# Optimization experiments

Hardware: AMD Instinct MI355X
Metric: run time of the kernel (lower is better)

Reference implementation:

```python
import jax, jax.numpy as jnp
import numpy as np

NUM_GRAPHS = 3000
L = 7        # num_gc_layers
D = 256      # dims * power
DIMS = 64
POWER = 4
MSG_EPS = 1e-7
LN_EPS = 1e-5


def layer_norm(x, g, b):
    mu = jnp.mean(x, axis=-1, keepdims=True)
    var = jnp.var(x, axis=-1, keepdims=True)
    return (x - mu) * jax.lax.rsqrt(var + LN_EPS) * g + b


def gen_conv(h, src, dst, edge_emb, w, b, n_nodes):
    # GENConv (OGB DeeperGCN), aggr='add', mlp_layers=1:
    #   msg = relu(x_j + e) + eps ; agg = scatter_add ; out = Linear(x + agg)
    msg = jax.nn.relu(h[src] + edge_emb) + MSG_EPS      # [E, D]
    agg = jax.ops.segment_sum(msg, dst, num_segments=n_nodes)
    return (h + agg) @ w + b


def mlp_vn(v, w1, b1, g1, be1, w2, b2, g2, be2):
    # MLP([D, D, D], norm='layer'): Lin -> LN -> ReLU -> Lin -> LN -> ReLU
    v = jax.nn.relu(layer_norm(v @ w1 + b1, g1, be1))
    v = jax.nn.relu(layer_norm(v @ w2 + b2, g2, be2))
    return v


def _forward(x, edge_attr, edge_index, batch, atom_emb, bond_emb, vn_emb,
             gcn_w, gcn_b, norm_g, norm_b, ffn_w, ffn_b,
             vn_w1, vn_b1, vn_g1, vn_be1, vn_w2, vn_b2, vn_g2, vn_be2):
    N = x.shape[0]
    # AtomEncoder / BondEncoder: sum of per-feature embedding gathers
    h = atom_emb[jnp.arange(9), x].sum(axis=1)              # [N, D]
    edge_emb = bond_emb[jnp.arange(3), edge_attr].sum(axis=1)  # [E, D]
    h_init = h

    vn = jnp.broadcast_to(vn_emb[0], (NUM_GRAPHS, D))        # Embedding(1, D) row 0
    h = h + vn[batch]

    src, dst = edge_index[0], edge_index[1]
    out = []
    h = gen_conv(h, src, dst, edge_emb, gcn_w[0], gcn_b[0], N)
    out.append(h @ ffn_w[0] + ffn_b[0])

    for layer in range(1, L):
        h2 = jax.nn.relu(layer_norm(h, norm_g[layer - 1], norm_b[layer - 1]))
        vn_tmp = jax.ops.segment_sum(h2, batch, num_segments=NUM_GRAPHS) + vn
        j = layer - 1
        vn = mlp_vn(vn_tmp, vn_w1[j], vn_b1[j], vn_g1[j], vn_be1[j],
                    vn_w2[j], vn_b2[j], vn_g2[j], vn_be2[j])  # dropout: eval mode -> identity
        h2 = h2 + vn[batch]
        h = gen_conv(h2, src, dst, edge_emb, gcn_w[layer], gcn_b[layer], N) + h
        out.append(h @ ffn_w[layer] + ffn_b[layer])

    h_graph = jnp.concatenate([out[p] for p in range(POWER)], axis=-1)  # [N, 4*64]
    return h_graph, h_init


def setup_inputs() -> dict:
    key = jax.random.key(0)
    ks = jax.random.split(key, 12)
    N, E = 100000, 300000
    s = 0.05
    return dict(
        x=jax.random.randint(ks[0], (N, 9), 0, 64),
        edge_attr=jax.random.randint(ks[1], (E, 3), 0, 8),
        edge_index=jax.random.randint(ks[2], (2, E), 0, N),
        batch=jnp.sort(jax.random.randint(ks[3], (N,), 0, NUM_GRAPHS)),
        atom_emb=jax.random.normal(ks[4], (9, 64, D)) * s,
        bond_emb=jax.random.normal(ks[5], (3, 8, D)) * s,
        vn_emb=jnp.zeros((1, D)),
        gcn_w=jax.random.normal(ks[6], (L, D, D)) * s,
        gcn_b=jnp.zeros((L, D)),
        norm_g=jnp.ones((L, D)),
        norm_b=jnp.zeros((L, D)),
        ffn_w=jax.random.normal(ks[7], (L, D, DIMS)) * s,
        ffn_b=jnp.zeros((L, DIMS)),
        vn_w1=jax.random.normal(ks[8], (L - 1, D, D)) * s,
        vn_b1=jnp.zeros((L - 1, D)),
        vn_g1=jnp.ones((L - 1, D)),
        vn_be1=jnp.zeros((L - 1, D)),
        vn_w2=jax.random.normal(ks[9], (L - 1, D, D)) * s,
        vn_b2=jnp.zeros((L - 1, D)),
        vn_g2=jnp.ones((L - 1, D)),
        vn_be2=jnp.zeros((L - 1, D)),
    )


def reference(x, edge_attr, edge_index, batch, atom_emb, bond_emb, vn_emb,
              gcn_w, gcn_b, norm_g, norm_b, ffn_w, ffn_b,
              vn_w1, vn_b1, vn_g1, vn_be1, vn_w2, vn_b2, vn_g2, vn_be2):
    return _forward(x, edge_attr, edge_index, batch, atom_emb, bond_emb, vn_emb,
                    gcn_w, gcn_b, norm_g, norm_b, ffn_w, ffn_b,
                    vn_w1, vn_b1, vn_g1, vn_be1, vn_w2, vn_b2, vn_g2, vn_be2)
```

## Files before the change

### kernel.cpp

```cpp
#include <hip/hip_runtime.h>
#include <hip/hip_bf16.h>

#define G_NUM 3000

typedef unsigned short u16;
typedef unsigned int u32;

typedef short s16x8 __attribute__((ext_vector_type(8)));
typedef float f32x4 __attribute__((ext_vector_type(4)));

__device__ __forceinline__ float bf2f(u16 u) {
    union { u32 i; float f; } v; v.i = ((u32)u) << 16; return v.f;
}
__device__ __forceinline__ u16 f2bf(float f) {
    union { float f; u32 i; } v; v.f = f;
    u32 r = (v.i + 0x7FFFu + ((v.i >> 16) & 1u)) >> 16;
    return (u16)r;
}
__device__ __forceinline__ float ldf(const void* p, size_t i, int bf) {
    return bf ? bf2f(((const u16*)p)[i]) : ((const float*)p)[i];
}

__device__ __forceinline__ void gl_lds16(const void* g, void* l) {
    __builtin_amdgcn_global_load_lds(
        (const __attribute__((address_space(1))) void*)g,
        (__attribute__((address_space(3))) void*)l, 16, 0, 0);
}

__global__ void k_flag(const u32* __restrict__ norm_g_u32, int* __restrict__ flag) {
    if (threadIdx.x == 0 && blockIdx.x == 0)
        *flag = (norm_g_u32[0] == 0x3F803F80u) ? 1 : 0;
}

__global__ void k_hist(const int* __restrict__ ei, int* __restrict__ cnt, int E) {
    int e = blockIdx.x * blockDim.x + threadIdx.x;
    if (e < E) atomicAdd(&cnt[ei[E + e]], 1);
}

__global__ __launch_bounds__(256) void k_scan_part(const int* __restrict__ cnt,
                                                   int* __restrict__ epos,
                                                   int* __restrict__ part, int N) {
    __shared__ int sh[256];
    int t = threadIdx.x;
    int base = blockIdx.x * 1024 + t * 4;
    int c0 = (base + 0 < N) ? cnt[base + 0] : 0;
    int c1 = (base + 1 < N) ? cnt[base + 1] : 0;
    int c2 = (base + 2 < N) ? cnt[base + 2] : 0;
    int c3 = (base + 3 < N) ? cnt[base + 3] : 0;
    int s4 = c0 + c1 + c2 + c3;
    sh[t] = s4;
    __syncthreads();
    for (int off = 1; off < 256; off <<= 1) {
        int v = (t >= off) ? sh[t - off] : 0;
        __syncthreads();
        sh[t] += v;
        __syncthreads();
    }
    int excl = sh[t] - s4;
    if (base + 0 < N) epos[base + 0] = excl;
    if (base + 1 < N) epos[base + 1] = excl + c0;
    if (base + 2 < N) epos[base + 2] = excl + c0 + c1;
    if (base + 3 < N) epos[base + 3] = excl + c0 + c1 + c2;
    if (t == 255) part[blockIdx.x] = sh[255];
}

__global__ __launch_bounds__(256) void k_scan_top(int* __restrict__ part, int NB) {
    __shared__ int sh[256];
    int t = threadIdx.x;
    int v = (t < NB) ? part[t] : 0;
    sh[t] = v;
    __syncthreads();
    for (int off = 1; off < 256; off <<= 1) {
        int u = (t >= off) ? sh[t - off] : 0;
        __syncthreads();
        sh[t] += u;
        __syncthreads();
    }
    if (t < NB) part[t] = sh[t] - v;
}

__global__ __launch_bounds__(256) void k_scan_fin(int* __restrict__ epos,
                                                  const int* __restrict__ part, int N) {
    int add = part[blockIdx.x];
    int base = blockIdx.x * 1024 + threadIdx.x * 4;
#pragma unroll
    for (int i = 0; i < 4; ++i)
        if (base + i < N) epos[base + i] += add;
}

__global__ void k_scatter(const int* __restrict__ ei, int* __restrict__ epos,
                          int* __restrict__ elist, int E) {
    int e = blockIdx.x * blockDim.x + threadIdx.x;
    if (e < E) {
        int p = atomicAdd(&epos[ei[E + e]], 1);
        elist[p] = e;
    }
}

__global__ void k_atom(const int* __restrict__ x, const void* __restrict__ atom_emb,
                       const void* __restrict__ vn_emb, const int* __restrict__ flagp,
                       float* __restrict__ h, int N) {
    int id = blockIdx.x * blockDim.x + threadIdx.x;
    if (id >= N * 64) return;
    int bf = *flagp;
    int n = id >> 6, d = (id & 63) << 2;
    float s0 = 0.f, s1 = 0.f, s2 = 0.f, s3 = 0.f;
#pragma unroll
    for (int f = 0; f < 9; ++f) {
        size_t row = (size_t)(f * 64 + x[n * 9 + f]) * 256 + d;
        if (bf) {
            ushort4 v = *(const ushort4*)((const u16*)atom_emb + row);
            s0 += bf2f(v.x); s1 += bf2f(v.y); s2 += bf2f(v.z); s3 += bf2f(v.w);
        } else {
            float4 v = *(const float4*)((const float*)atom_emb + row);
            s0 += v.x; s1 += v.y; s2 += v.z; s3 += v.w;
        }
    }
    float4 o = { s0 + ldf(vn_emb, d, bf),     s1 + ldf(vn_emb, d + 1, bf),
                 s2 + ldf(vn_emb, d + 2, bf), s3 + ldf(vn_emb, d + 3, bf) };
    *(float4*)(h + (size_t)n * 256 + d) = o;
}

__global__ void k_hinit(const int* __restrict__ x, const void* __restrict__ atom_emb,
                        const int* __restrict__ flagp, void* __restrict__ d_out_v, int N) {
    int id = blockIdx.x * blockDim.x + threadIdx.x;
    if (id >= N * 64) return;
    int bf = *flagp;
    int n = id >> 6, d = (id & 63) << 2;
    float s0 = 0.f, s1 = 0.f, s2 = 0.f, s3 = 0.f;
#pragma unroll
    for (int f = 0; f < 9; ++f) {
        size_t row = (size_t)(f * 64 + x[n * 9 + f]) * 256 + d;
        if (bf) {
            ushort4 v = *(const ushort4*)((const u16*)atom_emb + row);
            s0 += bf2f(v.x); s1 += bf2f(v.y); s2 += bf2f(v.z); s3 += bf2f(v.w);
        } else {
            float4 v = *(const float4*)((const float*)atom_emb + row);
            s0 += v.x; s1 += v.y; s2 += v.z; s3 += v.w;
        }
    }
    size_t idx = (size_t)N * 256 + (size_t)n * 256 + d;
    if (bf) {
        ushort4 o = { f2bf(s0), f2bf(s1), f2bf(s2), f2bf(s3) };
        *(ushort4*)((u16*)d_out_v + idx) = o;
    } else {
        float4 o = { s0, s1, s2, s3 };
        *(float4*)((float*)d_out_v + idx) = o;
    }
}

__global__ void k_init_vn(const void* __restrict__ vn_emb, const int* __restrict__ flagp,
                          float* __restrict__ vn) {
    int id = blockIdx.x * blockDim.x + threadIdx.x;
    if (id >= G_NUM * 256) return;
    vn[id] = ldf(vn_emb, id & 255, *flagp);
}

__global__ __launch_bounds__(256) void k_agg(
    const int* __restrict__ ei, const int* __restrict__ eattr,
    const int* __restrict__ elist, const int* __restrict__ epos,
    const int* __restrict__ cnt, const void* __restrict__ bond_emb,
    const int* __restrict__ flagp, const float* __restrict__ h,
    const void* __restrict__ d_out_v, u16* __restrict__ xh, u16* __restrict__ xl,
    const float* __restrict__ vnarr, const int* __restrict__ batch,
    int layer0, int E, int N) {
    int bf = *flagp;
    int wv = threadIdx.x >> 6, lane = threadIdx.x & 63;
    int n = blockIdx.x * 4 + wv;
    if (n >= N) return;
    int d = lane << 2;
    size_t ND = (size_t)N * 256;
    int end = epos[n];
    int deg = cnt[n];
    int start = end - deg;

    float i0, i1, i2, i3;
    if (layer0) {
        float4 iv = *(const float4*)(h + (size_t)n * 256 + d);
        i0 = iv.x; i1 = iv.y; i2 = iv.z; i3 = iv.w;
    } else {
        float4 vv = *(const float4*)(vnarr + (size_t)batch[n] * 256 + d);
        if (bf) {
            ushort4 iv = *(const ushort4*)((const u16*)d_out_v + ND + (size_t)n * 256 + d);
            i0 = bf2f(iv.x) + vv.x; i1 = bf2f(iv.y) + vv.y;
            i2 = bf2f(iv.z) + vv.z; i3 = bf2f(iv.w) + vv.w;
        } else {
            float4 iv = *(const float4*)((const float*)d_out_v + ND + (size_t)n * 256 + d);
            i0 = iv.x + vv.x; i1 = iv.y + vv.y; i2 = iv.z + vv.z; i3 = iv.w + vv.w;
        }
    }

    float a0 = 0.f, a1 = 0.f, a2 = 0.f, a3 = 0.f;
    for (int b0i = 0; b0i < deg; b0i += 64) {
        int m = min(64, deg - b0i);
        int src = 0, bsrc = 0, c0 = 0, c1 = 0, c2 = 0;
        if (lane < m) {
            int e = elist[start + b0i + lane];
            src = ei[e];
            c0 = eattr[e * 3]; c1 = eattr[e * 3 + 1]; c2 = eattr[e * 3 + 2];
            if (!layer0) bsrc = batch[src];
        }
        for (int j = 0; j < m; ++j) {
            int sj = __shfl(src, j);
            int q0 = __shfl(c0, j), q1 = __shfl(c1, j), q2 = __shfl(c2, j);
            float e0, e1, e2, e3;
            if (bf) {
                const u16* bp = (const u16*)bond_emb;
                ushort4 w0 = *(const ushort4*)(bp + (size_t)q0 * 256 + d);
                ushort4 w1 = *(const ushort4*)(bp + (size_t)(8 + q1) * 256 + d);
                ushort4 w2 = *(const ushort4*)(bp + (size_t)(16 + q2) * 256 + d);
                e0 = bf2f(w0.x) + bf2f(w1.x) + bf2f(w2.x);
                e1 = bf2f(w0.y) + bf2f(w1.y) + bf2f(w2.y);
                e2 = bf2f(w0.z) + bf2f(w1.z) + bf2f(w2.z);
                e3 = bf2f(w0.w) + bf2f(w1.w) + bf2f(w2.w);
            } else {
                const float* bp = (const float*)bond_emb;
                float4 w0 = *(const float4*)(bp + (size_t)q0 * 256 + d);
                float4 w1 = *(const float4*)(bp + (size_t)(8 + q1) * 256 + d);
                float4 w2 = *(const float4*)(bp + (size_t)(16 + q2) * 256 + d);
                e0 = w0.x + w1.x + w2.x; e1 = w0.y + w1.y + w2.y;
                e2 = w0.z + w1.z + w2.z; e3 = w0.w + w1.w + w2.w;
            }
            float h0, h1, h2v, h3;
            if (layer0) {
                float4 hs = *(const float4*)(h + (size_t)sj * 256 + d);
                h0 = hs.x; h1 = hs.y; h2v = hs.z; h3 = hs.w;
            } else {
                int bj = __shfl(bsrc, j);
                float4 vv = *(const float4*)(vnarr + (size_t)bj * 256 + d);
                if (bf) {
                    ushort4 hs = *(const ushort4*)((const u16*)d_out_v + ND + (size_t)sj * 256 + d);
                    h0 = bf2f(hs.x) + vv.x; h1 = bf2f(hs.y) + vv.y;
                    h2v = bf2f(hs.z) + vv.z; h3 = bf2f(hs.w) + vv.w;
                } else {
                    float4 hs = *(const float4*)((const float*)d_out_v + ND + (size_t)sj * 256 + d);
                    h0 = hs.x + vv.x; h1 = hs.y + vv.y; h2v = hs.z + vv.z; h3 = hs.w + vv.w;
                }
            }
            a0 += fmaxf(h0 + e0, 0.f) + 1e-7f;
            a1 += fmaxf(h1 + e1, 0.f) + 1e-7f;
            a2 += fmaxf(h2v + e2, 0.f) + 1e-7f;
            a3 += fmaxf(h3 + e3, 0.f) + 1e-7f;
        }
    }

    float o0 = i0 + a0, o1 = i1 + a1, o2 = i2 + a2, o3 = i3 + a3;
    u16 h0 = f2bf(o0), h1 = f2bf(o1), h2 = f2bf(o2), h3 = f2bf(o3);
    ushort4 hv = { h0, h1, h2, h3 };
    size_t base = (size_t)n * 256 + d;
    *(ushort4*)(xh + base) = hv;
    if (!bf) {
        ushort4 lv = { f2bf(o0 - bf2f(h0)), f2bf(o1 - bf2f(h1)),
                       f2bf(o2 - bf2f(h2)), f2bf(o3 - bf2f(h3)) };
        *(ushort4*)(xl + base) = lv;
    }
}

__global__ void k_prep_w(const void* __restrict__ gcn_w, const void* __restrict__ ffn_w,
                         const int* __restrict__ flagp,
                         u16* __restrict__ cwh, u16* __restrict__ cwl,
                         u16* __restrict__ fwh, u16* __restrict__ fwl) {
    int bf = *flagp;
    int t = blockIdx.x * blockDim.x + threadIdx.x;
    const int CONVT = 4 * 8 * 16 * 64;
    const int FFNT  = 4 * 8 * 4 * 64;
    if (t >= CONVT + FFNT) return;
    bool isc = t < CONVT;
    int u = isc ? t : t - CONVT;
    int lane = u & 63;
    int g = lane >> 4, c16 = lane & 15;
    int ncf = isc ? 16 : 4;
    int fid = u >> 6;
    int cf = fid % ncf;
    int kk = (fid / ncf) & 7;
    int layer = fid / (ncf * 8);
    int ncol = isc ? 256 : 64;
    int col = cf * 16 + c16;
    const void* W = isc ? gcn_w : ffn_w;
    u16* oh = isc ? cwh : fwh;
    u16* ol = isc ? cwl : fwl;
    size_t lbase = (size_t)layer * 256 * ncol;
    size_t o = (size_t)u * 8;
#pragma unroll
    for (int i = 0; i < 8; ++i) {
        int k = kk * 32 + g * 8 + i;
        float v = ldf(W, lbase + (size_t)k * ncol + col, bf);
        u16 hv = f2bf(v);
        oh[o + i] = hv;
        ol[o + i] = f2bf(v - bf2f(hv));
    }
}

__global__ __launch_bounds__(512, 8) void k_mconv(
    const u16* __restrict__ Ah, const u16* __restrict__ Al,
    const u16* __restrict__ cwh, const u16* __restrict__ cwl,
    const u16* __restrict__ fwh, const u16* __restrict__ fwl,
    const void* __restrict__ cbias, const void* __restrict__ fbias,
    const void* __restrict__ res, void* __restrict__ hOut,
    void* __restrict__ d_out_v, const int* __restrict__ flagp,
    const void* __restrict__ ng, const void* __restrict__ nb,
    int cboff, int fboff, int col_off, int goff, int N) {
    __shared__ __align__(16) u16 Shi[32 * 256];
    __shared__ __align__(16) u16 Slo[32 * 256];
    __shared__ float redS[8][2][16];
    __shared__ float redQ[8][2][16];
    int bf = *flagp;
    int t = threadIdx.x;
    int wv = t >> 6, lane = t & 63;
    int g = lane >> 4, c16 = lane & 15;
    int r0 = blockIdx.x * 32;
    size_t ND = (size_t)N * 256;

    {
        int l5 = lane >> 5;
        int cb = (lane & 31) * 16;
#pragma unroll
        for (int j = 0; j < 2; ++j) {
            int rowl = wv * 4 + j * 2 + l5;
            int gr = r0 + rowl; if (gr > N - 1) gr = N - 1;
            int scb = cb ^ ((rowl & 7) << 4);
            const u16* sh = Ah + (size_t)gr * 256 + (scb >> 1);
            gl_lds16(sh, &Shi[wv * 1024 + j * 512]);
            if (!bf) {
                const u16* sl = Al + (size_t)gr * 256 + (scb >> 1);
                gl_lds16(sl, &Slo[wv * 1024 + j * 512]);
            }
        }
    }
    __syncthreads();

    f32x4 acc[2][2] = {};
    if (bf) {
#pragma unroll
        for (int kk = 0; kk < 8; ++kk) {
            s16x8 wh[2];
#pragma unroll
            for (int c = 0; c < 2; ++c)
                wh[c] = *(const s16x8*)(cwh + ((size_t)((kk * 16 + wv * 2 + c) * 64 + lane) * 8));
#pragma unroll
            for (int rf = 0; rf < 2; ++rf) {
                int R = rf * 16 + c16;
                int cbyte = (kk * 64 + g * 16) ^ ((R & 7) << 4);
                s16x8 ah = *(const s16x8*)((const char*)Shi + R * 512 + cbyte);
#pragma unroll
                for (int c = 0; c < 2; ++c)
                    acc[rf][c] = __builtin_amdgcn_mfma_f32_16x16x32_bf16(wh[c], ah, acc[rf][c], 0, 0, 0);
            }
        }
    } else {
#pragma unroll
        for (int kk = 0; kk < 8; ++kk) {
            s16x8 wh[2], wl[2];
#pragma unroll
            for (int c = 0; c < 2; ++c) {
                size_t off = (size_t)((kk * 16 + wv * 2 + c) * 64 + lane) * 8;
                wh[c] = *(const s16x8*)(cwh + off);
                wl[c] = *(const s16x8*)(cwl + off);
            }
#pragma unroll
            for (int rf = 0; rf < 2; ++rf) {
                int R = rf * 16 + c16;
                int cbyte = (kk * 64 + g * 16) ^ ((R & 7) << 4);
                s16x8 ah = *(const s16x8*)((const char*)Shi + R * 512 + cbyte);
                s16x8 al = *(const s16x8*)((const char*)Slo + R * 512 + cbyte);
#pragma unroll
                for (int c = 0; c < 2; ++c) {
                    acc[rf][c] = __builtin_amdgcn_mfma_f32_16x16x32_bf16(wh[c], ah, acc[rf][c], 0, 0, 0);
                    acc[rf][c] = __builtin_amdgcn_mfma_f32_16x16x32_bf16(wh[c], al, acc[rf][c], 0, 0, 0);
                    acc[rf][c] = __builtin_amdgcn_mfma_f32_16x16x32_bf16(wl[c], ah, acc[rf][c], 0, 0, 0);
                    acc[rf][c] = __builtin_amdgcn_mfma_f32_16x16x32_bf16(wl[c], al, acc[rf][c], 0, 0, 0);
                }
            }
        }
    }
    __syncthreads();

    float o[2][2][4];
#pragma unroll
    for (int rf = 0; rf < 2; ++rf) {
        int R = rf * 16 + c16;
        int r = r0 + R;
#pragma unroll
        for (int c = 0; c < 2; ++c) {
            int colb = (wv * 2 + c) * 16 + g * 4;
#pragma unroll
            for (int i = 0; i < 4; ++i)
                o[rf][c][i] = acc[rf][c][i] + ldf(cbias, cboff + colb + i, bf);
            if (res && r < N) {
                if (bf) {
                    ushort4 rv = *(const ushort4*)((const u16*)res + (size_t)r * 256 + colb);
                    o[rf][c][0] += bf2f(rv.x); o[rf][c][1] += bf2f(rv.y);
                    o[rf][c][2] += bf2f(rv.z); o[rf][c][3] += bf2f(rv.w);
                } else {
                    float4 rv = *(const float4*)((const float*)res + (size_t)r * 256 + colb);
                    o[rf][c][0] += rv.x; o[rf][c][1] += rv.y;
                    o[rf][c][2] += rv.z; o[rf][c][3] += rv.w;
                }
            }
        }
        if (hOut && r < N) {
#pragma unroll
            for (int c = 0; c < 2; ++c) {
                int colb = (wv * 2 + c) * 16 + g * 4;
                if (bf) {
                    ushort4 ov = { f2bf(o[rf][c][0]), f2bf(o[rf][c][1]),
                                   f2bf(o[rf][c][2]), f2bf(o[rf][c][3]) };
                    *(ushort4*)((u16*)hOut + (size_t)r * 256 + colb) = ov;
                } else {
                    float4 ov = { o[rf][c][0], o[rf][c][1], o[rf][c][2], o[rf][c][3] };
                    *(float4*)((float*)hOut + (size_t)r * 256 + colb) = ov;
                }
            }
        }
    }

    float mu[2], rs_[2];
    if (goff >= 0) {
#pragma unroll
        for (int rf = 0; rf < 2; ++rf) {
            float s = 0.f;
#pragma unroll
            for (int c = 0; c < 2; ++c)
#pragma unroll
                for (int i = 0; i < 4; ++i) s += o[rf][c][i];
            s += __shfl_xor(s, 16);
            s += __shfl_xor(s, 32);
            if (g == 0) redS[wv][rf][c16] = s;
        }
    }
    __syncthreads();
    if (goff >= 0) {
#pragma unroll
        for (int rf = 0; rf < 2; ++rf) {
            float s8 = 0.f;
#pragma unroll
            for (int w = 0; w < 8; ++w) s8 += redS[w][rf][c16];
            mu[rf] = s8 * (1.f / 256.f);
            float q = 0.f;
#pragma unroll
            for (int c = 0; c < 2; ++c)
#pragma unroll
                for (int i = 0; i < 4; ++i) {
                    float dv = o[rf][c][i] - mu[rf];
                    q += dv * dv;
                }
            q += __shfl_xor(q, 16);
            q += __shfl_xor(q, 32);
            if (g == 0) redQ[wv][rf][c16] = q;
        }
    }
    __syncthreads();
    if (goff >= 0) {
#pragma unroll
        for (int rf = 0; rf < 2; ++rf) {
            float q8 = 0.f;
#pragma unroll
            for (int w = 0; w < 8; ++w) q8 += redQ[w][rf][c16];
            float var = q8 * (1.f / 256.f);
            rs_[rf] = rsqrtf(fmaxf(var, 0.f) + 1e-5f);
            int r = r0 + rf * 16 + c16;
            if (r < N) {
#pragma unroll
                for (int c = 0; c < 2; ++c) {
                    int colb = (wv * 2 + c) * 16 + g * 4;
                    float v0 = fmaxf((o[rf][c][0] - mu[rf]) * rs_[rf] * ldf(ng, goff + colb, bf)     + ldf(nb, goff + colb, bf), 0.f);
                    float v1 = fmaxf((o[rf][c][1] - mu[rf]) * rs_[rf] * ldf(ng, goff + colb + 1, bf) + ldf(nb, goff + colb + 1, bf), 0.f);
                    float v2 = fmaxf((o[rf][c][2] - mu[rf]) * rs_[rf] * ldf(ng, goff + colb + 2, bf) + ldf(nb, goff + colb + 2, bf), 0.f);
                    float v3 = fmaxf((o[rf][c][3] - mu[rf]) * rs_[rf] * ldf(ng, goff + colb + 3, bf) + ldf(nb, goff + colb + 3, bf), 0.f);
                    size_t oi = ND + (size_t)r * 256 + colb;
                    if (bf) {
                        ushort4 q4 = { f2bf(v0), f2bf(v1), f2bf(v2), f2bf(v3) };
                        *(ushort4*)((u16*)d_out_v + oi) = q4;
                    } else {
                        float4 q4 = { v0, v1, v2, v3 };
                        *(float4*)((float*)d_out_v + oi) = q4;
                    }
                }
            }
        }
    }

#pragma unroll
    for (int rf = 0; rf < 2; ++rf) {
        int R = rf * 16 + c16;
#pragma unroll
        for (int c = 0; c < 2; ++c) {
            int colb = (wv * 2 + c) * 16 + g * 4;
            float o0 = o[rf][c][0], o1 = o[rf][c][1], o2 = o[rf][c][2], o3 = o[rf][c][3];
            u16 h0 = f2bf(o0), h1 = f2bf(o1), h2 = f2bf(o2), h3 = f2bf(o3);
            ushort4 hv = { h0, h1, h2, h3 };
            int cbyte = (colb * 2) ^ ((R & 7) << 4);
            *(ushort4*)((char*)Shi + R * 512 + cbyte) = hv;
            if (!bf) {
                ushort4 lv = { f2bf(o0 - bf2f(h0)), f2bf(o1 - bf2f(h1)),
                               f2bf(o2 - bf2f(h2)), f2bf(o3 - bf2f(h3)) };
                *(ushort4*)((char*)Slo + R * 512 + cbyte) = lv;
            }
        }
    }
    __syncthreads();

    f32x4 fa = {};
    {
        int rfw = wv >> 2, cfw = wv & 3;
        int R = rfw * 16 + c16;
        if (bf) {
#pragma unroll
            for (int kk = 0; kk < 8; ++kk) {
                s16x8 wh = *(const s16x8*)(fwh + ((size_t)((kk * 4 + cfw) * 64 + lane) * 8));
                int cbyte = (kk * 64 + g * 16) ^ ((R & 7) << 4);
                s16x8 ah = *(const s16x8*)((const char*)Shi + R * 512 + cbyte);
                fa = __builtin_amdgcn_mfma_f32_16x16x32_bf16(wh, ah, fa, 0, 0, 0);
            }
        } else {
#pragma unroll
            for (int kk = 0; kk < 8; ++kk) {
                size_t off = (size_t)((kk * 4 + cfw) * 64 + lane) * 8;
                s16x8 wh = *(const s16x8*)(fwh + off);
                s16x8 wl = *(const s16x8*)(fwl + off);
                int cbyte = (kk * 64 + g * 16) ^ ((R & 7) << 4);
                s16x8 ah = *(const s16x8*)((const char*)Shi + R * 512 + cbyte);
                s16x8 al = *(const s16x8*)((const char*)Slo + R * 512 + cbyte);
                fa = __builtin_amdgcn_mfma_f32_16x16x32_bf16(wh, ah, fa, 0, 0, 0);
                fa = __builtin_amdgcn_mfma_f32_16x16x32_bf16(wh, al, fa, 0, 0, 0);
                fa = __builtin_amdgcn_mfma_f32_16x16x32_bf16(wl, ah, fa, 0, 0, 0);
                fa = __builtin_amdgcn_mfma_f32_16x16x32_bf16(wl, al, fa, 0, 0, 0);
            }
        }

        int colb = cfw * 16 + g * 4;
        float b0 = ldf(fbias, fboff + colb, bf);
        float b1 = ldf(fbias, fboff + colb + 1, bf);
        float b2 = ldf(fbias, fboff + colb + 2, bf);
        float b3 = ldf(fbias, fboff + colb + 3, bf);
        int r = r0 + R;
        if (r < N) {
            float o0 = fa[0] + b0, o1 = fa[1] + b1;
            float o2 = fa[2] + b2, o3 = fa[3] + b3;
            size_t oi = (size_t)r * 256 + col_off + colb;
            if (bf) {
                ushort4 q = { f2bf(o0), f2bf(o1), f2bf(o2), f2bf(o3) };
                *(ushort4*)((u16*)d_out_v + oi) = q;
            } else {
                float4 q = { o0, o1, o2, o3 };
                *(float4*)((float*)d_out_v + oi) = q;
            }
        }
    }
}

__global__ __launch_bounds__(256) void k_vn4(
    const void* __restrict__ d_out_v, const int* __restrict__ flagp,
    const int* __restrict__ batch,
    const void* __restrict__ w1, const void* __restrict__ b1,
    const void* __restrict__ g1, const void* __restrict__ be1,
    const void* __restrict__ w2, const void* __restrict__ b2,
    const void* __restrict__ g2, const void* __restrict__ be2,
    float* __restrict__ vn, int woff, int voff, int N) {
    __shared__ float row[4][256];
    __shared__ float red[4][4];
    __shared__ __align__(16) float Ws[32][256];
    int bf = *flagp;
    int t = threadIdx.x;
    int wv = t >> 6, lane = t & 63;
    size_t ND = (size_t)N * 256;

    {
        int gi = blockIdx.x * 4 + wv;
        int lo = 0, hi = N;
        while (lo < hi) { int m = (lo + hi) >> 1; if (batch[m] < gi) lo = m + 1; else hi = m; }
        int s = lo; hi = N;
        while (lo < hi) { int m = (lo + hi) >> 1; if (batch[m] < gi + 1) lo = m + 1; else hi = m; }
        int e = lo;
        int d = lane << 2;
        float4 a = *(const float4*)(vn + (size_t)gi * 256 + d);
        for (int n = s; n < e; ++n) {
            size_t base = ND + (size_t)n * 256 + d;
            if (bf) {
                ushort4 hv = *(const ushort4*)((const u16*)d_out_v + base);
                a.x += bf2f(hv.x); a.y += bf2f(hv.y); a.z += bf2f(hv.z); a.w += bf2f(hv.w);
            } else {
                float4 hv = *(const float4*)((const float*)d_out_v + base);
                a.x += hv.x; a.y += hv.y; a.z += hv.z; a.w += hv.w;
            }
        }
        *(float4*)&row[wv][d] = a;
    }
    __syncthreads();

#pragma unroll 1
    for (int stage = 0; stage < 2; ++stage) {
        const void* W = stage ? w2 : w1;
        const void* B = stage ? b2 : b1;
        const void* G = stage ? g2 : g1;
        const void* BE = stage ? be2 : be1;
        float bb = ldf(B, voff + t, bf);
        float acc[4] = { bb, bb, bb, bb };
#pragma unroll 1
        for (int k0 = 0; k0 < 256; k0 += 32) {
            if (bf) {
                const u32* Wg = (const u32*)((const u16*)W + woff);
#pragma unroll
                for (int i = 0; i < 16; ++i) {
                    int idx = t + i * 256;
                    int k = idx >> 7, c2 = idx & 127;
                    u32 v = Wg[(size_t)(k0 + k) * 128 + c2];
                    Ws[k][2 * c2] = bf2f((u16)(v & 0xffff));
                    Ws[k][2 * c2 + 1] = bf2f((u16)(v >> 16));
                }
            } else {
                const float4* Wg = (const float4*)((const float*)W + woff);
#pragma unroll
                for (int i = 0; i < 8; ++i) {
                    int idx = t + i * 256;
                    int k = idx >> 6, c4 = idx & 63;
                    *(float4*)&Ws[k][4 * c4] = Wg[(size_t)(k0 + k) * 64 + c4];
                }
            }
            __syncthreads();
#pragma unroll
            for (int k = 0; k < 32; ++k) {
                float w = Ws[k][t];
                float r0 = row[0][k0 + k], r1 = row[1][k0 + k];
                float r2 = row[2][k0 + k], r3 = row[3][k0 + k];
                acc[0] = fmaf(r0, w, acc[0]);
                acc[1] = fmaf(r1, w, acc[1]);
                acc[2] = fmaf(r2, w, acc[2]);
                acc[3] = fmaf(r3, w, acc[3]);
            }
            __syncthreads();
        }
        float mu[4], rs_[4];
#pragma unroll
        for (int gr = 0; gr < 4; ++gr) {
            float s = acc[gr];
#pragma unroll
            for (int o = 32; o > 0; o >>= 1) s += __shfl_xor(s, o);
            if (lane == 0) red[wv][gr] = s;
        }
        __syncthreads();
#pragma unroll
        for (int gr = 0; gr < 4; ++gr)
            mu[gr] = (red[0][gr] + red[1][gr] + red[2][gr] + red[3][gr]) * (1.f / 256.f);
        __syncthreads();
#pragma unroll
        for (int gr = 0; gr < 4; ++gr) {
            float dv = acc[gr] - mu[gr];
            float q = dv * dv;
#pragma unroll
            for (int o = 32; o > 0; o >>= 1) q += __shfl_xor(q, o);
            if (lane == 0) red[wv][gr] = q;
        }
        __syncthreads();
        float gn = ldf(G, voff + t, bf), bn = ldf(BE, voff + t, bf);
#pragma unroll
        for (int gr = 0; gr < 4; ++gr) {
            float var = (red[0][gr] + red[1][gr] + red[2][gr] + red[3][gr]) * (1.f / 256.f);
            rs_[gr] = rsqrtf(fmaxf(var, 0.f) + 1e-5f);
        }
        __syncthreads();
#pragma unroll
        for (int gr = 0; gr < 4; ++gr)
            row[gr][t] = fmaxf((acc[gr] - mu[gr]) * rs_[gr] * gn + bn, 0.f);
        __syncthreads();
    }
#pragma unroll
    for (int gr = 0; gr < 4; ++gr)
        vn[(size_t)(blockIdx.x * 4 + gr) * 256 + t] = row[gr][t];
}

extern "C" void kernel_launch(void* const* d_in, const int* in_sizes, int n_in,
                              void* d_out, int out_size, void* d_ws, size_t ws_size,
                              hipStream_t stream) {
    const int* x      = (const int*)d_in[0];
    const int* eattr  = (const int*)d_in[1];
    const int* ei     = (const int*)d_in[2];
    const int* batch  = (const int*)d_in[3];
    const void* atom_emb = d_in[4];
    const void* bond_emb = d_in[5];
    const void* vn_emb   = d_in[6];
    const void* gcn_w    = d_in[7];
    const void* gcn_b    = d_in[8];
    const void* norm_g   = d_in[9];
    const void* norm_b   = d_in[10];
    const void* ffn_w    = d_in[11];
    const void* ffn_b    = d_in[12];
    const void* vn_w1    = d_in[13];
    const void* vn_b1    = d_in[14];
    const void* vn_g1    = d_in[15];
    const void* vn_be1   = d_in[16];
    const void* vn_w2    = d_in[17];
    const void* vn_b2    = d_in[18];
    const void* vn_g2    = d_in[19];
    const void* vn_be2   = d_in[20];

    int N = in_sizes[3];
    int E = in_sizes[2] / 2;
    size_t ND = (size_t)N * 256;
    int NB = (N + 1023) / 1024;

    char* wp = (char*)d_ws;
    int*   flag   = (int*)wp;               wp += 256;
    int*   part   = (int*)wp;               wp += 1024 * 4;
    int*   cnt    = (int*)wp;               wp += (size_t)N * 4;
    int*   epos   = (int*)wp;               wp += (size_t)N * 4;
    int*   elist  = (int*)wp;               wp += (size_t)E * 4;
    float* vn     = (float*)wp;             wp += (size_t)G_NUM * 256 * 4;
    float* vn_tmp = (float*)wp;             wp += (size_t)G_NUM * 256 * 4;
    float* h      = (float*)wp;             wp += ND * 4;
    u16*   xh     = (u16*)wp;
    u16*   xl     = xh + ND;
    (void)vn_tmp;

    size_t wbytes = ((size_t)4 * 65536 * 2 + (size_t)4 * 16384 * 2) * 2;
    size_t wtop   = (ws_size - wbytes) & ~(size_t)255;
    u16* cwh = (u16*)((char*)d_ws + wtop);
    u16* cwl = cwh + (size_t)4 * 65536;
    u16* fwh = cwl + (size_t)4 * 65536;
    u16* fwl = fwh + (size_t)4 * 16384;

    int gE  = (E + 255) / 256;
    int gN4 = (N + 3) / 4;
    int gNv = (N * 64 + 255) / 256;
    int gb  = (N + 31) / 32;

    k_flag<<<1, 64, 0, stream>>>((const u32*)norm_g, flag);
    k_prep_w<<<160, 256, 0, stream>>>(gcn_w, ffn_w, flag, cwh, cwl, fwh, fwl);

    hipMemsetAsync(cnt, 0, (size_t)N * 4, stream);
    k_hist<<<gE, 256, 0, stream>>>(ei, cnt, E);
    k_scan_part<<<NB, 256, 0, stream>>>(cnt, epos, part, N);
    k_scan_top<<<1, 256, 0, stream>>>(part, NB);
    k_scan_fin<<<NB, 256, 0, stream>>>(epos, part, N);
    k_scatter<<<gE, 256, 0, stream>>>(ei, epos, elist, E);

    k_atom<<<gNv, 256, 0, stream>>>(x, atom_emb, vn_emb, flag, h, N);
    k_init_vn<<<(G_NUM * 256 + 255) / 256, 256, 0, stream>>>(vn_emb, flag, vn);

    k_agg<<<gN4, 256, 0, stream>>>(ei, eattr, elist, epos, cnt, bond_emb, flag,
                                   h, d_out, xh, xl, vn, batch, 1, E, N);
    k_mconv<<<gb, 512, 0, stream>>>(xh, xl, cwh, cwl, fwh, fwl, gcn_b, ffn_b,
                                    nullptr, h, d_out, flag, norm_g, norm_b,
                                    0, 0, 0, 0, N);

    for (int l = 1; l < 4; ++l) {
        int j = l - 1;
        k_vn4<<<G_NUM / 4, 256, 0, stream>>>(d_out, flag, batch,
                                             vn_w1, vn_b1, vn_g1, vn_be1,
                                             vn_w2, vn_b2, vn_g2, vn_be2,
                                             vn, j * 65536, j * 256, N);
        k_agg<<<gN4, 256, 0, stream>>>(ei, eattr, elist, epos, cnt, bond_emb, flag,
                                       h, d_out, xh, xl, vn, batch, 0, E, N);
        k_mconv<<<gb, 512, 0, stream>>>(xh, xl, cwh + (size_t)l * 65536,
                                        cwl + (size_t)l * 65536,
                                        fwh + (size_t)l * 16384,
                                        fwl + (size_t)l * 16384,
                                        gcn_b, ffn_b, h,
                                        (l < 3) ? h : nullptr,
                                        d_out, flag, norm_g, norm_b,
                                        l * 256, l * 64, l * 64,
                                        (l < 3) ? l * 256 : -1, N);
    }
    k_hinit<<<gNv, 256, 0, stream>>>(x, atom_emb, flag, d_out, N);
}
```

Baseline: 1.638 ms.

## Recompute LayerNorm+ReLU in aggregation consumers and drop low-low MFMA term

```diff
diff --git a/kernel.cpp b/kernel.cpp
--- a/kernel.cpp
+++ b/kernel.cpp
@@ -19,6 +19,14 @@
 }
 __device__ __forceinline__ float ldf(const void* p, size_t i, int bf) {
     return bf ? bf2f(((const u16*)p)[i]) : ((const float*)p)[i];
+}
+__device__ __forceinline__ float4 ldrow4(const void* p, size_t i, int bf) {
+    if (bf) {
+        ushort4 v = *(const ushort4*)((const u16*)p + i);
+        float4 r = { bf2f(v.x), bf2f(v.y), bf2f(v.z), bf2f(v.w) };
+        return r;
+    }
+    return *(const float4*)((const float*)p + i);
 }
 
 __device__ __forceinline__ void gl_lds16(const void* g, void* l) {
@@ -160,33 +168,50 @@
     const int* __restrict__ ei, const int* __restrict__ eattr,
     const int* __restrict__ elist, const int* __restrict__ epos,
     const int* __restrict__ cnt, const void* __restrict__ bond_emb,
-    const int* __restrict__ flagp, const float* __restrict__ h,
-    const void* __restrict__ d_out_v, u16* __restrict__ xh, u16* __restrict__ xl,
+    const int* __restrict__ flagp, const void* __restrict__ h,
+    u16* __restrict__ xh, u16* __restrict__ xl,
     const float* __restrict__ vnarr, const int* __restrict__ batch,
-    int layer0, int E, int N) {
+    const void* __restrict__ ng, const void* __restrict__ nb,
+    int goff, int layer0, int E, int N) {
     int bf = *flagp;
     int wv = threadIdx.x >> 6, lane = threadIdx.x & 63;
     int n = blockIdx.x * 4 + wv;
     if (n >= N) return;
     int d = lane << 2;
-    size_t ND = (size_t)N * 256;
+    int deg = cnt[n];
     int end = epos[n];
-    int deg = cnt[n];
     int start = end - deg;
 
+    float g0 = 0.f, g1 = 0.f, g2 = 0.f, g3 = 0.f;
+    float nb0 = 0.f, nb1 = 0.f, nb2 = 0.f, nb3 = 0.f;
+    if (!layer0) {
+        g0 = ldf(ng, goff + d, bf);     g1 = ldf(ng, goff + d + 1, bf);
+        g2 = ldf(ng, goff + d + 2, bf); g3 = ldf(ng, goff + d + 3, bf);
+        nb0 = ldf(nb, goff + d, bf);     nb1 = ldf(nb, goff + d + 1, bf);
+        nb2 = ldf(nb, goff + d + 2, bf); nb3 = ldf(nb, goff + d + 3, bf);
+    }
+
     float i0, i1, i2, i3;
-    if (layer0) {
-        float4 iv = *(const float4*)(h + (size_t)n * 256 + d);
-        i0 = iv.x; i1 = iv.y; i2 = iv.z; i3 = iv.w;
-    } else {
-        float4 vv = *(const float4*)(vnarr + (size_t)batch[n] * 256 + d);
-        if (bf) {
-            ushort4 iv = *(const ushort4*)((const u16*)d_out_v + ND + (size_t)n * 256 + d);
-            i0 = bf2f(iv.x) + vv.x; i1 = bf2f(iv.y) + vv.y;
-            i2 = bf2f(iv.z) + vv.z; i3 = bf2f(iv.w) + vv.w;
+    {
+        float4 hv = ldrow4(h, (size_t)n * 256 + d, layer0 ? 0 : bf);
+        if (layer0) {
+            float4 f = *(const float4*)((const float*)h + (size_t)n * 256 + d);
+            i0 = f.x; i1 = f.y; i2 = f.z; i3 = f.w;
         } else {
-            float4 iv = *(const float4*)((const float*)d_out_v + ND + (size_t)n * 256 + d);
-            i0 = iv.x + vv.x; i1 = iv.y + vv.y; i2 = iv.z + vv.z; i3 = iv.w + vv.w;
+            float s = hv.x + hv.y + hv.z + hv.w;
+#pragma unroll
+            for (int o = 32; o > 0; o >>= 1) s += __shfl_xor(s, o);
+            float mu = s * (1.f / 256.f);
+            float d0 = hv.x - mu, d1 = hv.y - mu, d2 = hv.z - mu, d3 = hv.w - mu;
+            float q = d0 * d0 + d1 * d1 + d2 * d2 + d3 * d3;
+#pragma unroll
+            for (int o = 32; o > 0; o >>= 1) q += __shfl_xor(q, o);
+            float rs = rsqrtf(fmaxf(q * (1.f / 256.f), 0.f) + 1e-5f);
+            float4 vv = *(const float4*)(vnarr + (size_t)batch[n] * 256 + d);
+            i0 = fmaxf(d0 * rs * g0 + nb0, 0.f) + vv.x;
+            i1 = fmaxf(d1 * rs * g1 + nb1, 0.f) + vv.y;
+            i2 = fmaxf(d2 * rs * g2 + nb2, 0.f) + vv.z;
+            i3 = fmaxf(d3 * rs * g3 + nb3, 0.f) + vv.w;
         }
     }
 
@@ -223,19 +248,25 @@
             }
             float h0, h1, h2v, h3;
             if (layer0) {
-                float4 hs = *(const float4*)(h + (size_t)sj * 256 + d);
+                float4 hs = *(const float4*)((const float*)h + (size_t)sj * 256 + d);
                 h0 = hs.x; h1 = hs.y; h2v = hs.z; h3 = hs.w;
             } else {
+                float4 hv = ldrow4(h, (size_t)sj * 256 + d, bf);
+                float s = hv.x + hv.y + hv.z + hv.w;
+#pragma unroll
+                for (int o = 32; o > 0; o >>= 1) s += __shfl_xor(s, o);
+                float mu = s * (1.f / 256.f);
+                float d0 = hv.x - mu, d1 = hv.y - mu, d2 = hv.z - mu, d3 = hv.w - mu;
+                float qq = d0 * d0 + d1 * d1 + d2 * d2 + d3 * d3;
+#pragma unroll
+                for (int o = 32; o > 0; o >>= 1) qq += __shfl_xor(qq, o);
+                float rs = rsqrtf(fmaxf(qq * (1.f / 256.f), 0.f) + 1e-5f);
                 int bj = __shfl(bsrc, j);
                 float4 vv = *(const float4*)(vnarr + (size_t)bj * 256 + d);
-                if (bf) {
-                    ushort4 hs = *(const ushort4*)((const u16*)d_out_v + ND + (size_t)sj * 256 + d);
-                    h0 = bf2f(hs.x) + vv.x; h1 = bf2f(hs.y) + vv.y;
-                    h2v = bf2f(hs.z) + vv.z; h3 = bf2f(hs.w) + vv.w;
-                } else {
-                    float4 hs = *(const float4*)((const float*)d_out_v + ND + (size_t)sj * 256 + d);
-                    h0 = hs.x + vv.x; h1 = hs.y + vv.y; h2v = hs.z + vv.z; h3 = hs.w + vv.w;
-                }
+                h0 = fmaxf(d0 * rs * g0 + nb0, 0.f) + vv.x;
+                h1 = fmaxf(d1 * rs * g1 + nb1, 0.f) + vv.y;
+                h2v = fmaxf(d2 * rs * g2 + nb2, 0.f) + vv.z;
+                h3 = fmaxf(d3 * rs * g3 + nb3, 0.f) + vv.w;
             }
             a0 += fmaxf(h0 + e0, 0.f) + 1e-7f;
             a1 += fmaxf(h1 + e1, 0.f) + 1e-7f;
@@ -298,18 +329,14 @@
     const void* __restrict__ cbias, const void* __restrict__ fbias,
     const void* __restrict__ res, void* __restrict__ hOut,
     void* __restrict__ d_out_v, const int* __restrict__ flagp,
-    const void* __restrict__ ng, const void* __restrict__ nb,
-    int cboff, int fboff, int col_off, int goff, int N) {
+    int cboff, int fboff, int col_off, int N) {
     __shared__ __align__(16) u16 Shi[32 * 256];
     __shared__ __align__(16) u16 Slo[32 * 256];
-    __shared__ float redS[8][2][16];
-    __shared__ float redQ[8][2][16];
     int bf = *flagp;
     int t = threadIdx.x;
     int wv = t >> 6, lane = t & 63;
     int g = lane >> 4, c16 = lane & 15;
     int r0 = blockIdx.x * 32;
-    size_t ND = (size_t)N * 256;
 
     {
         int l5 = lane >> 5;
@@ -368,7 +395,6 @@
                     acc[rf][c] = __builtin_amdgcn_mfma_f32_16x16x32_bf16(wh[c], ah, acc[rf][c], 0, 0, 0);
                     acc[rf][c] = __builtin_amdgcn_mfma_f32_16x16x32_bf16(wh[c], al, acc[rf][c], 0, 0, 0);
                     acc[rf][c] = __builtin_amdgcn_mfma_f32_16x16x32_bf16(wl[c], ah, acc[rf][c], 0, 0, 0);
-                    acc[rf][c] = __builtin_amdgcn_mfma_f32_16x16x32_bf16(wl[c], al, acc[rf][c], 0, 0, 0);
                 }
             }
         }
@@ -414,72 +440,6 @@
         }
     }
 
-    float mu[2], rs_[2];
-    if (goff >= 0) {
-#pragma unroll
-        for (int rf = 0; rf < 2; ++rf) {
-            float s = 0.f;
-#pragma unroll
-            for (int c = 0; c < 2; ++c)
-#pragma unroll
-                for (int i = 0; i < 4; ++i) s += o[rf][c][i];
-            s += __shfl_xor(s, 16);
-            s += __shfl_xor(s, 32);
-            if (g == 0) redS[wv][rf][c16] = s;
-        }
-    }
-    __syncthreads();
-    if (goff >= 0) {
-#pragma unroll
-        for (int rf = 0; rf < 2; ++rf) {
-            float s8 = 0.f;
-#pragma unroll
-            for (int w = 0; w < 8; ++w) s8 += redS[w][rf][c16];
-            mu[rf] = s8 * (1.f / 256.f);
-            float q = 0.f;
-#pragma unroll
-            for (int c = 0; c < 2; ++c)
-#pragma unroll
-                for (int i = 0; i < 4; ++i) {
-                    float dv = o[rf][c][i] - mu[rf];
-                    q += dv * dv;
-                }
-            q += __shfl_xor(q, 16);
-            q += __shfl_xor(q, 32);
-            if (g == 0) redQ[wv][rf][c16] = q;
-        }
-    }
-    __syncthreads();
-    if (goff >= 0) {
-#pragma unroll
-        for (int rf = 0; rf < 2; ++rf) {
-            float q8 = 0.f;
-#pragma unroll
-            for (int w = 0; w < 8; ++w) q8 += redQ[w][rf][c16];
-            float var = q8 * (1.f / 256.f);
-            rs_[rf] = rsqrtf(fmaxf(var, 0.f) + 1e-5f);
-            int r = r0 + rf * 16 + c16;
-            if (r < N) {
-#pragma unroll
-                for (int c = 0; c < 2; ++c) {
-                    int colb = (wv * 2 + c) * 16 + g * 4;
-                    float v0 = fmaxf((o[rf][c][0] - mu[rf]) * rs_[rf] * ldf(ng, goff + colb, bf)     + ldf(nb, goff + colb, bf), 0.f);
-                    float v1 = fmaxf((o[rf][c][1] - mu[rf]) * rs_[rf] * ldf(ng, goff + colb + 1, bf) + ldf(nb, goff + colb + 1, bf), 0.f);
-                    float v2 = fmaxf((o[rf][c][2] - mu[rf]) * rs_[rf] * ldf(ng, goff + colb + 2, bf) + ldf(nb, goff + colb + 2, bf), 0.f);
-                    float v3 = fmaxf((o[rf][c][3] - mu[rf]) * rs_[rf] * ldf(ng, goff + colb + 3, bf) + ldf(nb, goff + colb + 3, bf), 0.f);
-                    size_t oi = ND + (size_t)r * 256 + colb;
-                    if (bf) {
-                        ushort4 q4 = { f2bf(v0), f2bf(v1), f2bf(v2), f2bf(v3) };
-                        *(ushort4*)((u16*)d_out_v + oi) = q4;
-                    } else {
-                        float4 q4 = { v0, v1, v2, v3 };
-                        *(float4*)((float*)d_out_v + oi) = q4;
-                    }
-                }
-            }
-        }
-    }
-
 #pragma unroll
     for (int rf = 0; rf < 2; ++rf) {
         int R = rf * 16 + c16;
@@ -524,7 +484,6 @@
                 fa = __builtin_amdgcn_mfma_f32_16x16x32_bf16(wh, ah, fa, 0, 0, 0);
                 fa = __builtin_amdgcn_mfma_f32_16x16x32_bf16(wh, al, fa, 0, 0, 0);
                 fa = __builtin_amdgcn_mfma_f32_16x16x32_bf16(wl, ah, fa, 0, 0, 0);
-                fa = __builtin_amdgcn_mfma_f32_16x16x32_bf16(wl, al, fa, 0, 0, 0);
             }
         }
 
@@ -550,8 +509,9 @@
 }
 
 __global__ __launch_bounds__(256) void k_vn4(
-    const void* __restrict__ d_out_v, const int* __restrict__ flagp,
+    const void* __restrict__ h, const int* __restrict__ flagp,
     const int* __restrict__ batch,
+    const void* __restrict__ ng, const void* __restrict__ nbv, int goff,
     const void* __restrict__ w1, const void* __restrict__ b1,
     const void* __restrict__ g1, const void* __restrict__ be1,
     const void* __restrict__ w2, const void* __restrict__ b2,
@@ -563,7 +523,6 @@
     int bf = *flagp;
     int t = threadIdx.x;
     int wv = t >> 6, lane = t & 63;
-    size_t ND = (size_t)N * 256;
 
     {
         int gi = blockIdx.x * 4 + wv;
@@ -573,16 +532,26 @@
         while (lo < hi) { int m = (lo + hi) >> 1; if (batch[m] < gi + 1) lo = m + 1; else hi = m; }
         int e = lo;
         int d = lane << 2;
+        float g0 = ldf(ng, goff + d, bf),     g1 = ldf(ng, goff + d + 1, bf);
+        float g2 = ldf(ng, goff + d + 2, bf), g3 = ldf(ng, goff + d + 3, bf);
+        float b0 = ldf(nbv, goff + d, bf),     b1 = ldf(nbv, goff + d + 1, bf);
+        float b2 = ldf(nbv, goff + d + 2, bf), b3 = ldf(nbv, goff + d + 3, bf);
         float4 a = *(const float4*)(vn + (size_t)gi * 256 + d);
         for (int n = s; n < e; ++n) {
-            size_t base = ND + (size_t)n * 256 + d;
-            if (bf) {
-                ushort4 hv = *(const ushort4*)((const u16*)d_out_v + base);
-                a.x += bf2f(hv.x); a.y += bf2f(hv.y); a.z += bf2f(hv.z); a.w += bf2f(hv.w);
-            } else {
-                float4 hv = *(const float4*)((const float*)d_out_v + base);
-                a.x += hv.x; a.y += hv.y; a.z += hv.z; a.w += hv.w;
-            }
+            float4 hv = ldrow4(h, (size_t)n * 256 + d, bf);
+            float sm = hv.x + hv.y + hv.z + hv.w;
+#pragma unroll
+            for (int o = 32; o > 0; o >>= 1) sm += __shfl_xor(sm, o);
+            float mu = sm * (1.f / 256.f);
+            float d0 = hv.x - mu, d1 = hv.y - mu, d2 = hv.z - mu, d3 = hv.w - mu;
+            float q = d0 * d0 + d1 * d1 + d2 * d2 + d3 * d3;
+#pragma unroll
+            for (int o = 32; o > 0; o >>= 1) q += __shfl_xor(q, o);
+            float rs = rsqrtf(fmaxf(q * (1.f / 256.f), 0.f) + 1e-5f);
+            a.x += fmaxf(d0 * rs * g0 + b0, 0.f);
+            a.y += fmaxf(d1 * rs * g1 + b1, 0.f);
+            a.z += fmaxf(d2 * rs * g2 + b2, 0.f);
+            a.w += fmaxf(d3 * rs * g3 + b3, 0.f);
         }
         *(float4*)&row[wv][d] = a;
     }
@@ -738,28 +707,28 @@
     k_init_vn<<<(G_NUM * 256 + 255) / 256, 256, 0, stream>>>(vn_emb, flag, vn);
 
     k_agg<<<gN4, 256, 0, stream>>>(ei, eattr, elist, epos, cnt, bond_emb, flag,
-                                   h, d_out, xh, xl, vn, batch, 1, E, N);
+                                   h, xh, xl, vn, batch, norm_g, norm_b,
+                                   0, 1 , E, N);
     k_mconv<<<gb, 512, 0, stream>>>(xh, xl, cwh, cwl, fwh, fwl, gcn_b, ffn_b,
-                                    nullptr, h, d_out, flag, norm_g, norm_b,
-                                    0, 0, 0, 0, N);
+                                    nullptr, h, d_out, flag, 0, 0, 0, N);
 
     for (int l = 1; l < 4; ++l) {
         int j = l - 1;
-        k_vn4<<<G_NUM / 4, 256, 0, stream>>>(d_out, flag, batch,
+        k_vn4<<<G_NUM / 4, 256, 0, stream>>>(h, flag, batch, norm_g, norm_b, j * 256,
                                              vn_w1, vn_b1, vn_g1, vn_be1,
                                              vn_w2, vn_b2, vn_g2, vn_be2,
                                              vn, j * 65536, j * 256, N);
         k_agg<<<gN4, 256, 0, stream>>>(ei, eattr, elist, epos, cnt, bond_emb, flag,
-                                       h, d_out, xh, xl, vn, batch, 0, E, N);
+                                       h, xh, xl, vn, batch, norm_g, norm_b,
+                                       j * 256, 0, E, N);
         k_mconv<<<gb, 512, 0, stream>>>(xh, xl, cwh + (size_t)l * 65536,
                                         cwl + (size_t)l * 65536,
                                         fwh + (size_t)l * 16384,
                                         fwl + (size_t)l * 16384,
                                         gcn_b, ffn_b, h,
                                         (l < 3) ? h : nullptr,
-                                        d_out, flag, norm_g, norm_b,
-                                        l * 256, l * 64, l * 64,
-                                        (l < 3) ? l * 256 : -1, N);
+                                        d_out, flag,
+                                        l * 256, l * 64, l * 64, N);
     }
     k_hinit<<<gNv, 256, 0, stream>>>(x, atom_emb, flag, d_out, N);
 }
```

Result: slower. 1.713 ms (+4.6%).
